# Optimization experiments

Hardware: AMD Instinct MI355X
Metric: run time of the kernel (lower is better)

## Reference

```python
import jax, jax.numpy as jnp
import numpy as np

EMBED_DIM = 256
NUM_HEADS = 8
HEAD_DIM = EMBED_DIM // NUM_HEADS
FFN_DIM = 4 * EMBED_DIM
B, N = 2, 2048


def _layernorm(x, w, b, eps=1e-5):
    mu = jnp.mean(x, axis=-1, keepdims=True)
    var = jnp.var(x, axis=-1, keepdims=True)
    return (x - mu) * jax.lax.rsqrt(var + eps) * w + b


def setup_inputs() -> dict:
    key = jax.random.key(0)
    ks = jax.random.split(key, 16)
    s = 0.02
    d = {
        "x": jax.random.normal(ks[0], (B, N, EMBED_DIM), jnp.float32),
        "influence_matrix": jax.random.uniform(ks[1], (B, N, N), jnp.float32),
        "qw": jax.random.normal(ks[2], (EMBED_DIM, EMBED_DIM), jnp.float32) * s,
        "qb": jnp.zeros((EMBED_DIM,), jnp.float32),
        "kw": jax.random.normal(ks[3], (EMBED_DIM, EMBED_DIM), jnp.float32) * s,
        "kb": jnp.zeros((EMBED_DIM,), jnp.float32),
        "vw": jax.random.normal(ks[4], (EMBED_DIM, EMBED_DIM), jnp.float32) * s,
        "vb": jnp.zeros((EMBED_DIM,), jnp.float32),
        "ow": jax.random.normal(ks[5], (EMBED_DIM, EMBED_DIM), jnp.float32) * s,
        "ob": jnp.zeros((EMBED_DIM,), jnp.float32),
        "w1": jax.random.normal(ks[6], (EMBED_DIM, FFN_DIM), jnp.float32) * s,
        "b1": jnp.zeros((FFN_DIM,), jnp.float32),
        "w2": jax.random.normal(ks[7], (FFN_DIM, EMBED_DIM), jnp.float32) * s,
        "b2": jnp.zeros((EMBED_DIM,), jnp.float32),
        "ln1_w": jnp.ones((EMBED_DIM,), jnp.float32),
        "ln1_b": jnp.zeros((EMBED_DIM,), jnp.float32),
        "ln2_w": jnp.ones((EMBED_DIM,), jnp.float32),
        "ln2_b": jnp.zeros((EMBED_DIM,), jnp.float32),
    }
    return d


def reference(x, influence_matrix, qw, qb, kw, kb, vw, vb, ow, ob,
              w1, b1, w2, b2, ln1_w, ln1_b, ln2_w, ln2_b):
    # --- pre-norm attention with multiplicative influence bias ---
    h = _layernorm(x, ln1_w, ln1_b)
    q = (h @ qw + qb).reshape(B, N, NUM_HEADS, HEAD_DIM)
    k = (h @ kw + kb).reshape(B, N, NUM_HEADS, HEAD_DIM)
    v = (h @ vw + vb).reshape(B, N, NUM_HEADS, HEAD_DIM)
    scores = jnp.einsum('bnhd,bmhd->bhnm', q, k) / np.sqrt(HEAD_DIM).astype(np.float32)
    scores = scores * (1.0 + influence_matrix[:, None, :, :])  # multiplicative bias
    attn = jax.nn.softmax(scores, axis=-1)
    out = jnp.einsum('bhnm,bmhd->bnhd', attn, v).reshape(B, N, EMBED_DIM)
    x = x + out @ ow + ob
    # --- GELU FFN (torch GELU is exact erf form) ---
    h2 = _layernorm(x, ln2_w, ln2_b)
    ff = jax.nn.gelu(h2 @ w1 + b1, approximate=False) @ w2 + b2
    return x + ff
```

## Files before the change

### kernel.cpp

```cpp
#include <hip/hip_runtime.h>
#include <hip/hip_bf16.h>
#include <math.h>

#define NSEQ 2048
#define DMODEL 256
#define STRD 296

typedef __attribute__((ext_vector_type(8))) __bf16 bf16x8;
typedef __attribute__((ext_vector_type(4))) float f32x4;
typedef __attribute__((ext_vector_type(8))) unsigned short ushort8;
typedef __attribute__((ext_vector_type(4))) unsigned int uint4e;

__device__ __forceinline__ unsigned short f2b(float f) {
    return __builtin_bit_cast(unsigned short, (__bf16)f);
}
__device__ __forceinline__ float b2f(unsigned short u) {
    return (float)__builtin_bit_cast(__bf16, u);
}
__device__ __forceinline__ bf16x8 ldfrag16(const void* p) {
    return __builtin_bit_cast(bf16x8, *(const uint4e*)p);
}
__device__ __forceinline__ uint4e pack8(float a0,float a1,float a2,float a3,
                                        float b0,float b1,float b2,float b3) {
    uint4e u;
    u.x = (unsigned)f2b(a0) | ((unsigned)f2b(a1) << 16);
    u.y = (unsigned)f2b(a2) | ((unsigned)f2b(a3) << 16);
    u.z = (unsigned)f2b(b0) | ((unsigned)f2b(b1) << 16);
    u.w = (unsigned)f2b(b2) | ((unsigned)f2b(b3) << 16);
    return u;
}

__global__ __launch_bounds__(256)
void prep_kernel(const float* __restrict__ qw, const float* __restrict__ kw,
                 const float* __restrict__ vw, const float* __restrict__ ow,
                 const float* __restrict__ w1, const float* __restrict__ w2,
                 __bf16* __restrict__ qwT, __bf16* __restrict__ kwT,
                 __bf16* __restrict__ vwT, __bf16* __restrict__ owT,
                 __bf16* __restrict__ w1T, __bf16* __restrict__ w2T)
{
    __shared__ float tile[32][33];
    const int b = blockIdx.x;
    const float* in; __bf16* out; int K, N, k0, n0;
    if (b < 256) {
        const int wsel = b >> 6, tl = b & 63;
        in  = (wsel == 0) ? qw  : (wsel == 1) ? kw  : (wsel == 2) ? vw  : ow;
        out = (wsel == 0) ? qwT : (wsel == 1) ? kwT : (wsel == 2) ? vwT : owT;
        K = 256; N = 256; k0 = (tl >> 3) * 32; n0 = (tl & 7) * 32;
    } else if (b < 512) {
        const int tl = b - 256;
        in = w1; out = w1T; K = 256; N = 1024;
        k0 = (tl >> 5) * 32; n0 = (tl & 31) * 32;
    } else {
        const int tl = b - 512;
        in = w2; out = w2T; K = 1024; N = 256;
        k0 = (tl >> 3) * 32; n0 = (tl & 7) * 32;
    }
    const int tx = threadIdx.x & 31, ty = threadIdx.x >> 5;
#pragma unroll
    for (int j = 0; j < 4; ++j)
        tile[ty * 4 + j][tx] = in[(size_t)(k0 + ty * 4 + j) * N + n0 + tx];
    __syncthreads();
#pragma unroll
    for (int j = 0; j < 4; ++j)
        out[(size_t)(n0 + ty * 4 + j) * K + k0 + tx] = (__bf16)tile[tx][ty * 4 + j];
}

__device__ __forceinline__ void stage_panel(const __bf16* __restrict__ src, int ldk,
                                            int col0, int kbase, short* dst)
{
    const int t = threadIdx.x;
#pragma unroll
    for (int i = 0; i < 8; ++i) {
        const int flat = i * 256 + t;
        const int row = flat >> 5, seg = flat & 31;
        *(uint4e*)(dst + row * STRD + seg * 8) =
            *(const uint4e*)(src + (size_t)(col0 + row) * ldk + kbase + seg * 8);
    }
}

__device__ __forceinline__ void ln_to_lds(const float* __restrict__ xrow0,
                                          const float* __restrict__ lw,
                                          const float* __restrict__ lb, short* As)
{
    const int t = threadIdx.x;
    const int r = t >> 2, q = t & 3;
    const float* xp = xrow0 + (size_t)r * 256 + q * 64;
    float4 v[16];
    float s = 0.f, s2 = 0.f;
#pragma unroll
    for (int j = 0; j < 16; ++j) {
        v[j] = *(const float4*)(xp + j * 4);
        s  += v[j].x + v[j].y + v[j].z + v[j].w;
        s2 += v[j].x*v[j].x + v[j].y*v[j].y + v[j].z*v[j].z + v[j].w*v[j].w;
    }
    s  += __shfl_xor(s, 1);  s  += __shfl_xor(s, 2);
    s2 += __shfl_xor(s2, 1); s2 += __shfl_xor(s2, 2);
    const float mu = s * (1.0f / 256.0f);
    const float rs = rsqrtf(s2 * (1.0f / 256.0f) - mu * mu + 1e-5f);
    const float* gw = lw + q * 64;
    const float* gb = lb + q * 64;
#pragma unroll
    for (int j = 0; j < 8; ++j) {
        const float4 w0 = *(const float4*)(gw + j * 8);
        const float4 w1 = *(const float4*)(gw + j * 8 + 4);
        const float4 b0 = *(const float4*)(gb + j * 8);
        const float4 b1 = *(const float4*)(gb + j * 8 + 4);
        const float4 a = v[j * 2], bq = v[j * 2 + 1];
        *(uint4e*)(As + r * STRD + q * 64 + j * 8) = pack8(
            (a.x - mu) * rs * w0.x + b0.x, (a.y - mu) * rs * w0.y + b0.y,
            (a.z - mu) * rs * w0.z + b0.z, (a.w - mu) * rs * w0.w + b0.w,
            (bq.x - mu) * rs * w1.x + b1.x, (bq.y - mu) * rs * w1.y + b1.y,
            (bq.z - mu) * rs * w1.z + b1.z, (bq.w - mu) * rs * w1.w + b1.w);
    }
}

__global__ __launch_bounds__(256)
void qkv_kernel(const float* __restrict__ x,
                const float* __restrict__ lw, const float* __restrict__ lb,
                const __bf16* __restrict__ qwT, const __bf16* __restrict__ kwT,
                const __bf16* __restrict__ vwT,
                const float* __restrict__ qb, const float* __restrict__ kb,
                const float* __restrict__ vb,
                __bf16* __restrict__ qo, __bf16* __restrict__ ko,
                __bf16* __restrict__ vto)
{
    __shared__ short As[64 * STRD];
    __shared__ short Ws[64 * STRD];
    const int z = blockIdx.z;
    const __bf16* WT  = (z == 0) ? qwT : (z == 1) ? kwT : vwT;
    const float* bias = (z == 0) ? qb  : (z == 1) ? kb  : vb;
    const int row0 = blockIdx.y * 64, col0 = blockIdx.x * 64;

    ln_to_lds(x + (size_t)row0 * 256, lw, lb, As);
    stage_panel(WT, 256, col0, 0, Ws);
    __syncthreads();

    const int t = threadIdx.x, lane = t & 63, w = t >> 6;
    const int g = lane >> 4, c = lane & 15;
    const short* ap = As + (w * 16 + c) * STRD + g * 8;
    const short* bp = Ws + c * STRD + g * 8;
    f32x4 acc[4] = {};
#pragma unroll
    for (int kc = 0; kc < 256; kc += 32) {
        const bf16x8 a = ldfrag16(ap + kc);
#pragma unroll
        for (int dt = 0; dt < 4; ++dt) {
            const bf16x8 bb = ldfrag16(bp + dt * 16 * STRD + kc);
            acc[dt] = __builtin_amdgcn_mfma_f32_16x16x32_bf16(a, bb, acc[dt], 0, 0, 0);
        }
    }

    if (z == 2) {
        __syncthreads();
        short* LT = Ws;
#pragma unroll
        for (int dt = 0; dt < 4; ++dt)
#pragma unroll
        for (int r = 0; r < 4; ++r)
            LT[(dt * 16 + c) * 72 + w * 16 + g * 4 + r] =
                (short)f2b(acc[dt][r] + bias[col0 + dt * 16 + c]);
        __syncthreads();
        const int col = t >> 2;
#pragma unroll
        for (int i = 0; i < 2; ++i) {
            const int seg = (t & 3) * 2 + i;
            *(uint4e*)(vto + (size_t)(col0 + col) * 4096 + row0 + seg * 8) =
                *(const uint4e*)&LT[col * 72 + seg * 8];
        }
    } else {
        __bf16* o = (z == 0) ? qo : ko;
#pragma unroll
        for (int dt = 0; dt < 4; ++dt)
#pragma unroll
        for (int r = 0; r < 4; ++r) {
            const int row = row0 + w * 16 + g * 4 + r;
            const int col = col0 + dt * 16 + c;
            o[(size_t)row * 256 + col] = (__bf16)(acc[dt][r] + bias[col]);
        }
    }
}

__global__ __launch_bounds__(256)
void oproj_kernel(const __bf16* __restrict__ ao, const __bf16* __restrict__ owT,
                  const float* __restrict__ ob, const float* __restrict__ x,
                  float* __restrict__ x2)
{
    __shared__ short Ws[64 * STRD];
    const int row0 = blockIdx.y * 64, col0 = blockIdx.x * 64;
    stage_panel(owT, 256, col0, 0, Ws);
    __syncthreads();
    const int t = threadIdx.x, lane = t & 63, w = t >> 6;
    const int g = lane >> 4, c = lane & 15;
    const __bf16* arow = ao + (size_t)(row0 + w * 16 + c) * 256 + g * 8;
    const short* bp = Ws + c * STRD + g * 8;
    f32x4 acc[4] = {};
#pragma unroll
    for (int kc = 0; kc < 256; kc += 32) {
        const bf16x8 a = ldfrag16(arow + kc);
#pragma unroll
        for (int dt = 0; dt < 4; ++dt) {
            const bf16x8 bb = ldfrag16(bp + dt * 16 * STRD + kc);
            acc[dt] = __builtin_amdgcn_mfma_f32_16x16x32_bf16(a, bb, acc[dt], 0, 0, 0);
        }
    }
#pragma unroll
    for (int dt = 0; dt < 4; ++dt)
#pragma unroll
    for (int r = 0; r < 4; ++r) {
        const int row = row0 + w * 16 + g * 4 + r;
        const int col = col0 + dt * 16 + c;
        x2[(size_t)row * 256 + col] =
            x[(size_t)row * 256 + col] + acc[dt][r] + ob[col];
    }
}

__global__ __launch_bounds__(256)
void ffn1_kernel(const float* __restrict__ x2,
                 const float* __restrict__ lw, const float* __restrict__ lb,
                 const __bf16* __restrict__ w1T, const float* __restrict__ b1,
                 __bf16* __restrict__ ff)
{
    __shared__ short As[64 * STRD];
    __shared__ short Ws[64 * STRD];
    const int row0 = blockIdx.y * 64, col0 = blockIdx.x * 64;
    ln_to_lds(x2 + (size_t)row0 * 256, lw, lb, As);
    stage_panel(w1T, 256, col0, 0, Ws);
    __syncthreads();
    const int t = threadIdx.x, lane = t & 63, w = t >> 6;
    const int g = lane >> 4, c = lane & 15;
    const short* ap = As + (w * 16 + c) * STRD + g * 8;
    const short* bp = Ws + c * STRD + g * 8;
    f32x4 acc[4] = {};
#pragma unroll
    for (int kc = 0; kc < 256; kc += 32) {
        const bf16x8 a = ldfrag16(ap + kc);
#pragma unroll
        for (int dt = 0; dt < 4; ++dt) {
            const bf16x8 bb = ldfrag16(bp + dt * 16 * STRD + kc);
            acc[dt] = __builtin_amdgcn_mfma_f32_16x16x32_bf16(a, bb, acc[dt], 0, 0, 0);
        }
    }
#pragma unroll
    for (int dt = 0; dt < 4; ++dt)
#pragma unroll
    for (int r = 0; r < 4; ++r) {
        const int row = row0 + w * 16 + g * 4 + r;
        const int col = col0 + dt * 16 + c;
        float val = acc[dt][r] + b1[col];
        val = 0.5f * val * (1.0f + erff(val * 0.70710678118654752f));
        ff[(size_t)row * 1024 + col] = (__bf16)val;
    }
}

__global__ __launch_bounds__(256)
void ffn2_kernel(const __bf16* __restrict__ ff, const __bf16* __restrict__ w2T,
                 const float* __restrict__ b2, const float* __restrict__ x2,
                 float* __restrict__ out)
{
    __shared__ short Ws[64 * STRD];
    const int row0 = blockIdx.y * 64, col0 = blockIdx.x * 64;
    const int t = threadIdx.x, lane = t & 63, w = t >> 6;
    const int g = lane >> 4, c = lane & 15;
    const __bf16* arow = ff + (size_t)(row0 + w * 16 + c) * 1024 + g * 8;
    const short* bp = Ws + c * STRD + g * 8;
    f32x4 acc[4] = {};
    for (int ck = 0; ck < 4; ++ck) {
        if (ck) __syncthreads();
        stage_panel(w2T, 1024, col0, ck * 256, Ws);
        __syncthreads();
#pragma unroll
        for (int kc = 0; kc < 256; kc += 32) {
            const bf16x8 a = ldfrag16(arow + ck * 256 + kc);
#pragma unroll
            for (int dt = 0; dt < 4; ++dt) {
                const bf16x8 bb = ldfrag16(bp + dt * 16 * STRD + kc);
                acc[dt] = __builtin_amdgcn_mfma_f32_16x16x32_bf16(a, bb, acc[dt], 0, 0, 0);
            }
        }
    }
#pragma unroll
    for (int dt = 0; dt < 4; ++dt)
#pragma unroll
    for (int r = 0; r < 4; ++r) {
        const int row = row0 + w * 16 + g * 4 + r;
        const int col = col0 + dt * 16 + c;
        out[(size_t)row * 256 + col] =
            x2[(size_t)row * 256 + col] + acc[dt][r] + b2[col];
    }
}

__global__ __launch_bounds__(512, 4)
void attn_kernel(const __bf16* __restrict__ Q, const __bf16* __restrict__ K,
                 const __bf16* __restrict__ VT, const float* __restrict__ infl,
                 __bf16* __restrict__ Opart, float* __restrict__ ml)
{
    __shared__ float ilds[2][16][66];
    __shared__ short Pm[8][16][104];

    const int t    = threadIdx.x;
    const int lane = t & 63;
    const int w    = t >> 6;
    const int g    = lane >> 4, c = lane & 15;
    const int b    = blockIdx.z;
    const int sp   = blockIdx.y;
    const int n0   = blockIdx.x * 16;
    const int m_start = sp * 512;
    const float scale = 0.17677669529663687f;

    const bf16x8 qf = ldfrag16(Q + (size_t)(b * NSEQ + n0 + c) * DMODEL + w * 32 + g * 8);

    const __bf16* Khead = K  + (size_t)(b * NSEQ + c) * DMODEL + w * 32 + g * 8;
    const __bf16* Vhead = VT + (size_t)(w * 32 + c) * (2 * NSEQ) + b * NSEQ + g * 8;

    const int irN = t >> 5, icol = (t & 31) * 2;
    const float* iptr = infl + (size_t)(b * NSEQ + n0 + irN) * NSEQ + icol;

    f32x4 Oacc[2] = {};
    float lsum[4] = {0.f, 0.f, 0.f, 0.f};

    float2 ireg = *(const float2*)(iptr + m_start);
    bf16x8 kf[4];
#pragma unroll
    for (int dt = 0; dt < 4; ++dt)
        kf[dt] = ldfrag16(Khead + (size_t)(m_start + dt * 16) * DMODEL);

    int buf = 0;
    for (int it = 0; it < 8; ++it) {
        const int m0 = m_start + (it << 6);
        const int mn = m_start + (((it + 1) & 7) << 6);

        *(float2*)&ilds[buf][irN][icol] = ireg;
        asm volatile("s_waitcnt lgkmcnt(0)" ::: "memory");
        __builtin_amdgcn_s_barrier();

        ireg = *(const float2*)(iptr + mn);
        bf16x8 kn[4];
#pragma unroll
        for (int dt = 0; dt < 4; ++dt)
            kn[dt] = ldfrag16(Khead + (size_t)(mn + dt * 16) * DMODEL);
        bf16x8 vf[4];
#pragma unroll
        for (int ks = 0; ks < 2; ++ks)
#pragma unroll
            for (int dt = 0; dt < 2; ++dt)
                vf[ks * 2 + dt] =
                    ldfrag16(Vhead + (size_t)(dt * 16) * (2 * NSEQ) + m0 + ks * 32);

        f32x4 s[4];
#pragma unroll
        for (int mt = 0; mt < 4; ++mt) {
            f32x4 z4 = {0.f, 0.f, 0.f, 0.f};
            s[mt] = __builtin_amdgcn_mfma_f32_16x16x32_bf16(qf, kf[mt], z4, 0, 0, 0);
        }

        float p[4][4];
#pragma unroll
        for (int mt = 0; mt < 4; ++mt)
#pragma unroll
            for (int r = 0; r < 4; ++r) {
                const float iw = scale + scale * ilds[buf][g * 4 + r][mt * 16 + c];
                const float pe = __expf(s[mt][r] * iw);
                p[mt][r] = pe;
                lsum[r] += pe;
            }
#pragma unroll
        for (int mt = 0; mt < 4; ++mt)
#pragma unroll
            for (int r = 0; r < 4; ++r)
                Pm[w][g * 4 + r][mt * 16 + c] = (short)f2b(p[mt][r]);
        asm volatile("" ::: "memory");

#pragma unroll
        for (int ks = 0; ks < 2; ++ks) {
            const bf16x8 pf = ldfrag16(&Pm[w][c][ks * 32 + g * 8]);
            Oacc[0] = __builtin_amdgcn_mfma_f32_16x16x32_bf16(pf, vf[ks * 2 + 0], Oacc[0], 0, 0, 0);
            Oacc[1] = __builtin_amdgcn_mfma_f32_16x16x32_bf16(pf, vf[ks * 2 + 1], Oacc[1], 0, 0, 0);
        }

#pragma unroll
        for (int dt = 0; dt < 4; ++dt)
            kf[dt] = kn[dt];
        buf ^= 1;
    }

#pragma unroll
    for (int off = 1; off < 16; off <<= 1)
#pragma unroll
        for (int r = 0; r < 4; ++r)
            lsum[r] += __shfl_xor(lsum[r], off);

    if (c == 0) {
#pragma unroll
        for (int r = 0; r < 4; ++r)
            ml[((size_t)(sp * 4096 + b * NSEQ + n0 + g * 4 + r)) * 8 + w] = lsum[r];
    }

#pragma unroll
    for (int r = 0; r < 4; ++r) {
        const int grow = b * NSEQ + n0 + g * 4 + r;
#pragma unroll
        for (int dt = 0; dt < 2; ++dt)
            Opart[(size_t)(sp * 4096 + grow) * 256 + w * 32 + dt * 16 + c] =
                (__bf16)Oacc[dt][r];
    }
}

__global__ __launch_bounds__(256)
void combine_kernel(const __bf16* __restrict__ Opart, const float* __restrict__ ml,
                    __bf16* __restrict__ ao)
{
    const int tid = blockIdx.x * 256 + threadIdx.x;
    const int row = tid >> 5;
    const int d0  = (tid & 31) * 8;
    const int h   = d0 >> 5;
    float l = 0.f;
#pragma unroll
    for (int sp = 0; sp < 4; ++sp)
        l += ml[((size_t)(sp * 4096 + row)) * 8 + h];
    const float inv = 1.0f / l;
    float acc[8] = {};
#pragma unroll
    for (int sp = 0; sp < 4; ++sp) {
        const ushort8 xp = *(const ushort8*)(Opart + ((size_t)(sp * 4096 + row)) * 256 + d0);
#pragma unroll
        for (int e = 0; e < 8; ++e) acc[e] += b2f(xp[e]);
    }
    __bf16 o[8];
#pragma unroll
    for (int e = 0; e < 8; ++e) o[e] = (__bf16)(acc[e] * inv);
    *(uint4e*)(ao + (size_t)row * 256 + d0) = *(uint4e*)o;
}

extern "C" void kernel_launch(void* const* d_in, const int* in_sizes, int n_in,
                              void* d_out, int out_size, void* d_ws, size_t ws_size,
                              hipStream_t stream)
{
    (void)in_sizes; (void)n_in; (void)out_size; (void)ws_size;
    const float* x    = (const float*)d_in[0];
    const float* infl = (const float*)d_in[1];
    const float* qw   = (const float*)d_in[2];
    const float* qb   = (const float*)d_in[3];
    const float* kw   = (const float*)d_in[4];
    const float* kb   = (const float*)d_in[5];
    const float* vw   = (const float*)d_in[6];
    const float* vb   = (const float*)d_in[7];
    const float* ow   = (const float*)d_in[8];
    const float* ob_  = (const float*)d_in[9];
    const float* w1   = (const float*)d_in[10];
    const float* b1   = (const float*)d_in[11];
    const float* w2   = (const float*)d_in[12];
    const float* b2   = (const float*)d_in[13];
    const float* ln1w = (const float*)d_in[14];
    const float* ln1b = (const float*)d_in[15];
    const float* ln2w = (const float*)d_in[16];
    const float* ln2b = (const float*)d_in[17];
    float* out = (float*)d_out;

    char* ws = (char*)d_ws;
    __bf16* qwT   = (__bf16*)(ws);
    __bf16* kwT   = (__bf16*)(ws + (128u << 10));
    __bf16* vwT   = (__bf16*)(ws + (256u << 10));
    __bf16* owT   = (__bf16*)(ws + (384u << 10));
    __bf16* w1T   = (__bf16*)(ws + (512u << 10));
    __bf16* w2T   = (__bf16*)(ws + (1024u << 10));
    __bf16* q     = (__bf16*)(ws +  2 * 1048576ull);
    __bf16* kx    = (__bf16*)(ws +  4 * 1048576ull);
    __bf16* vt    = (__bf16*)(ws +  6 * 1048576ull);
    __bf16* Opart = (__bf16*)(ws +  8 * 1048576ull);
    float*  mlbuf = (float*) (ws + 16 * 1048576ull);
    __bf16* ao    = (__bf16*)(ws + 17 * 1048576ull);
    float*  x2    = (float*) (ws + 19 * 1048576ull);
    __bf16* ff    = (__bf16*)(ws + 23 * 1048576ull);

    prep_kernel<<<768, 256, 0, stream>>>(qw, kw, vw, ow, w1, w2,
                                         qwT, kwT, vwT, owT, w1T, w2T);
    qkv_kernel<<<dim3(4, 64, 3), 256, 0, stream>>>(x, ln1w, ln1b, qwT, kwT, vwT,
                                                   qb, kb, vb, q, kx, vt);
    attn_kernel<<<dim3(128, 4, 2), 512, 0, stream>>>(q, kx, vt, infl, Opart, mlbuf);
    combine_kernel<<<512, 256, 0, stream>>>(Opart, mlbuf, ao);
    oproj_kernel<<<dim3(4, 64), 256, 0, stream>>>(ao, owT, ob_, x, x2);
    ffn1_kernel<<<dim3(16, 64), 256, 0, stream>>>(x2, ln2w, ln2b, w1T, b1, ff);
    ffn2_kernel<<<dim3(4, 64), 256, 0, stream>>>(ff, w2T, b2, x2, out);
}
```

Measured before the change: 238.0 us.

## Restructure pipeline: standalone LayerNorm, head-major K/V, fused combine, split-K FFN2

LayerNorm moves out of the GEMM kernels. LN1 now runs inside the prep launch and LN2 in its own kernel, and both write bf16 activations. K and V^T are stored head-major so attention reads contiguous per-head tiles. Attention drops its shared-memory influence staging and barrier and reads influence values straight into registers, using one head per wave with 256-thread blocks. The softmax combine step is folded into the output projection, GEMM row tiles shrink to 32 to raise block counts, and FFN2 becomes split-K with a separate reduction kernel. The gain is more parallelism and fewer barriers, at the cost of extra launches and more partial-sum traffic.

New measurement: 218.8 us. 8.1% less time.

```diff
diff --git a/kernel.cpp b/kernel.cpp
--- a/kernel.cpp
+++ b/kernel.cpp
@@ -3,12 +3,13 @@
 #include <math.h>
 
 #define NSEQ 2048
-#define DMODEL 256
-#define STRD 296
+#define SW 264
+#define PS 104
 
 typedef __attribute__((ext_vector_type(8))) __bf16 bf16x8;
 typedef __attribute__((ext_vector_type(4))) float f32x4;
 typedef __attribute__((ext_vector_type(8))) unsigned short ushort8;
+typedef __attribute__((ext_vector_type(4))) unsigned short ushort4e;
 typedef __attribute__((ext_vector_type(4))) unsigned int uint4e;
 
 __device__ __forceinline__ unsigned short f2b(float f) {
@@ -20,38 +21,68 @@
 __device__ __forceinline__ bf16x8 ldfrag16(const void* p) {
     return __builtin_bit_cast(bf16x8, *(const uint4e*)p);
 }
-__device__ __forceinline__ uint4e pack8(float a0,float a1,float a2,float a3,
-                                        float b0,float b1,float b2,float b3) {
-    uint4e u;
-    u.x = (unsigned)f2b(a0) | ((unsigned)f2b(a1) << 16);
-    u.y = (unsigned)f2b(a2) | ((unsigned)f2b(a3) << 16);
-    u.z = (unsigned)f2b(b0) | ((unsigned)f2b(b1) << 16);
-    u.w = (unsigned)f2b(b2) | ((unsigned)f2b(b3) << 16);
-    return u;
+
+__device__ __forceinline__ void ln_row(const float* __restrict__ x,
+                                       const float* __restrict__ g,
+                                       const float* __restrict__ b,
+                                       __bf16* __restrict__ out, int row, int lane)
+{
+    const float4 v = *(const float4*)(x + (size_t)row * 256 + lane * 4);
+    float s  = v.x + v.y + v.z + v.w;
+    float s2 = v.x*v.x + v.y*v.y + v.z*v.z + v.w*v.w;
+#pragma unroll
+    for (int off = 32; off; off >>= 1) {
+        s  += __shfl_xor(s, off);
+        s2 += __shfl_xor(s2, off);
+    }
+    const float mu = s * (1.0f / 256.0f);
+    const float rs = rsqrtf(s2 * (1.0f / 256.0f) - mu * mu + 1e-5f);
+    const float4 gv = *(const float4*)(g + lane * 4);
+    const float4 bv = *(const float4*)(b + lane * 4);
+    ushort4e o4;
+    o4.x = f2b((v.x - mu) * rs * gv.x + bv.x);
+    o4.y = f2b((v.y - mu) * rs * gv.y + bv.y);
+    o4.z = f2b((v.z - mu) * rs * gv.z + bv.z);
+    o4.w = f2b((v.w - mu) * rs * gv.w + bv.w);
+    *(ushort4e*)(out + (size_t)row * 256 + lane * 4) = o4;
+}
+
+__global__ __launch_bounds__(256)
+void ln_kernel(const float* __restrict__ x, const float* __restrict__ g,
+               const float* __restrict__ b, __bf16* __restrict__ out)
+{
+    ln_row(x, g, b, out, blockIdx.x * 4 + (threadIdx.x >> 6), threadIdx.x & 63);
 }
 
 __global__ __launch_bounds__(256)
 void prep_kernel(const float* __restrict__ qw, const float* __restrict__ kw,
                  const float* __restrict__ vw, const float* __restrict__ ow,
                  const float* __restrict__ w1, const float* __restrict__ w2,
+                 const float* __restrict__ x,
+                 const float* __restrict__ ln1w, const float* __restrict__ ln1b,
                  __bf16* __restrict__ qwT, __bf16* __restrict__ kwT,
                  __bf16* __restrict__ vwT, __bf16* __restrict__ owT,
-                 __bf16* __restrict__ w1T, __bf16* __restrict__ w2T)
+                 __bf16* __restrict__ w1T, __bf16* __restrict__ w2T,
+                 __bf16* __restrict__ h)
 {
     __shared__ float tile[32][33];
-    const int b = blockIdx.x;
+    const int bid = blockIdx.x;
+    if (bid >= 768) {
+        ln_row(x, ln1w, ln1b, h, (bid - 768) * 4 + (threadIdx.x >> 6), threadIdx.x & 63);
+        return;
+    }
     const float* in; __bf16* out; int K, N, k0, n0;
-    if (b < 256) {
-        const int wsel = b >> 6, tl = b & 63;
+    if (bid < 256) {
+        const int wsel = bid >> 6, tl = bid & 63;
         in  = (wsel == 0) ? qw  : (wsel == 1) ? kw  : (wsel == 2) ? vw  : ow;
         out = (wsel == 0) ? qwT : (wsel == 1) ? kwT : (wsel == 2) ? vwT : owT;
         K = 256; N = 256; k0 = (tl >> 3) * 32; n0 = (tl & 7) * 32;
-    } else if (b < 512) {
-        const int tl = b - 256;
+    } else if (bid < 512) {
+        const int tl = bid - 256;
         in = w1; out = w1T; K = 256; N = 1024;
         k0 = (tl >> 5) * 32; n0 = (tl & 31) * 32;
     } else {
-        const int tl = b - 512;
+        const int tl = bid - 512;
         in = w2; out = w2T; K = 1024; N = 256;
         k0 = (tl >> 3) * 32; n0 = (tl & 7) * 32;
     }
@@ -73,362 +104,312 @@
     for (int i = 0; i < 8; ++i) {
         const int flat = i * 256 + t;
         const int row = flat >> 5, seg = flat & 31;
-        *(uint4e*)(dst + row * STRD + seg * 8) =
+        *(uint4e*)(dst + row * SW + seg * 8) =
             *(const uint4e*)(src + (size_t)(col0 + row) * ldk + kbase + seg * 8);
     }
 }
 
-__device__ __forceinline__ void ln_to_lds(const float* __restrict__ xrow0,
-                                          const float* __restrict__ lw,
-                                          const float* __restrict__ lb, short* As)
-{
-    const int t = threadIdx.x;
-    const int r = t >> 2, q = t & 3;
-    const float* xp = xrow0 + (size_t)r * 256 + q * 64;
-    float4 v[16];
-    float s = 0.f, s2 = 0.f;
-#pragma unroll
-    for (int j = 0; j < 16; ++j) {
-        v[j] = *(const float4*)(xp + j * 4);
-        s  += v[j].x + v[j].y + v[j].z + v[j].w;
-        s2 += v[j].x*v[j].x + v[j].y*v[j].y + v[j].z*v[j].z + v[j].w*v[j].w;
-    }
-    s  += __shfl_xor(s, 1);  s  += __shfl_xor(s, 2);
-    s2 += __shfl_xor(s2, 1); s2 += __shfl_xor(s2, 2);
-    const float mu = s * (1.0f / 256.0f);
-    const float rs = rsqrtf(s2 * (1.0f / 256.0f) - mu * mu + 1e-5f);
-    const float* gw = lw + q * 64;
-    const float* gb = lb + q * 64;
-#pragma unroll
-    for (int j = 0; j < 8; ++j) {
-        const float4 w0 = *(const float4*)(gw + j * 8);
-        const float4 w1 = *(const float4*)(gw + j * 8 + 4);
-        const float4 b0 = *(const float4*)(gb + j * 8);
-        const float4 b1 = *(const float4*)(gb + j * 8 + 4);
-        const float4 a = v[j * 2], bq = v[j * 2 + 1];
-        *(uint4e*)(As + r * STRD + q * 64 + j * 8) = pack8(
-            (a.x - mu) * rs * w0.x + b0.x, (a.y - mu) * rs * w0.y + b0.y,
-            (a.z - mu) * rs * w0.z + b0.z, (a.w - mu) * rs * w0.w + b0.w,
-            (bq.x - mu) * rs * w1.x + b1.x, (bq.y - mu) * rs * w1.y + b1.y,
-            (bq.z - mu) * rs * w1.z + b1.z, (bq.w - mu) * rs * w1.w + b1.w);
-    }
-}
-
-__global__ __launch_bounds__(256)
-void qkv_kernel(const float* __restrict__ x,
-                const float* __restrict__ lw, const float* __restrict__ lb,
+__global__ __launch_bounds__(256)
+void qkv_kernel(const __bf16* __restrict__ h,
                 const __bf16* __restrict__ qwT, const __bf16* __restrict__ kwT,
                 const __bf16* __restrict__ vwT,
                 const float* __restrict__ qb, const float* __restrict__ kb,
                 const float* __restrict__ vb,
-                __bf16* __restrict__ qo, __bf16* __restrict__ ko,
-                __bf16* __restrict__ vto)
-{
-    __shared__ short As[64 * STRD];
-    __shared__ short Ws[64 * STRD];
+                __bf16* __restrict__ qo, __bf16* __restrict__ khm,
+                __bf16* __restrict__ vthm)
+{
+    __shared__ short Ws[64 * SW];
     const int z = blockIdx.z;
     const __bf16* WT  = (z == 0) ? qwT : (z == 1) ? kwT : vwT;
     const float* bias = (z == 0) ? qb  : (z == 1) ? kb  : vb;
-    const int row0 = blockIdx.y * 64, col0 = blockIdx.x * 64;
-
-    ln_to_lds(x + (size_t)row0 * 256, lw, lb, As);
+    const int row0 = blockIdx.y * 32, col0 = blockIdx.x * 64;
     stage_panel(WT, 256, col0, 0, Ws);
     __syncthreads();
-
     const int t = threadIdx.x, lane = t & 63, w = t >> 6;
+    const int wr = w & 1, wc = w >> 1;
     const int g = lane >> 4, c = lane & 15;
-    const short* ap = As + (w * 16 + c) * STRD + g * 8;
-    const short* bp = Ws + c * STRD + g * 8;
-    f32x4 acc[4] = {};
+    const __bf16* arow = h + (size_t)(row0 + wr * 16 + c) * 256 + g * 8;
+    const short* bp = Ws + (wc * 32 + c) * SW + g * 8;
+    f32x4 acc[2] = {};
 #pragma unroll
     for (int kc = 0; kc < 256; kc += 32) {
-        const bf16x8 a = ldfrag16(ap + kc);
-#pragma unroll
-        for (int dt = 0; dt < 4; ++dt) {
-            const bf16x8 bb = ldfrag16(bp + dt * 16 * STRD + kc);
-            acc[dt] = __builtin_amdgcn_mfma_f32_16x16x32_bf16(a, bb, acc[dt], 0, 0, 0);
-        }
-    }
-
+        const bf16x8 a  = ldfrag16(arow + kc);
+        const bf16x8 b0 = ldfrag16(bp + kc);
+        const bf16x8 b1 = ldfrag16(bp + 16 * SW + kc);
+        acc[0] = __builtin_amdgcn_mfma_f32_16x16x32_bf16(a, b0, acc[0], 0, 0, 0);
+        acc[1] = __builtin_amdgcn_mfma_f32_16x16x32_bf16(a, b1, acc[1], 0, 0, 0);
+    }
+    const int bb = row0 >> 11, nl0 = row0 & 2047;
     if (z == 2) {
         __syncthreads();
         short* LT = Ws;
 #pragma unroll
-        for (int dt = 0; dt < 4; ++dt)
-#pragma unroll
-        for (int r = 0; r < 4; ++r)
-            LT[(dt * 16 + c) * 72 + w * 16 + g * 4 + r] =
-                (short)f2b(acc[dt][r] + bias[col0 + dt * 16 + c]);
+        for (int ch = 0; ch < 2; ++ch)
+#pragma unroll
+        for (int r = 0; r < 4; ++r) {
+            const int cl = wc * 32 + ch * 16 + c;
+            LT[cl * 40 + wr * 16 + g * 4 + r] = (short)f2b(acc[ch][r] + bias[col0 + cl]);
+        }
         __syncthreads();
-        const int col = t >> 2;
-#pragma unroll
-        for (int i = 0; i < 2; ++i) {
-            const int seg = (t & 3) * 2 + i;
-            *(uint4e*)(vto + (size_t)(col0 + col) * 4096 + row0 + seg * 8) =
-                *(const uint4e*)&LT[col * 72 + seg * 8];
-        }
+        const int cl = t >> 2, seg = t & 3;
+        const int C = col0 + cl;
+        *(uint4e*)(vthm + ((size_t)((bb * 8 + (C >> 5)) * 32 + (C & 31))) * NSEQ + nl0 + seg * 8) =
+            *(const uint4e*)&LT[cl * 40 + seg * 8];
     } else {
-        __bf16* o = (z == 0) ? qo : ko;
-#pragma unroll
-        for (int dt = 0; dt < 4; ++dt)
+#pragma unroll
+        for (int ch = 0; ch < 2; ++ch)
 #pragma unroll
         for (int r = 0; r < 4; ++r) {
-            const int row = row0 + w * 16 + g * 4 + r;
-            const int col = col0 + dt * 16 + c;
-            o[(size_t)row * 256 + col] = (__bf16)(acc[dt][r] + bias[col]);
-        }
-    }
-}
-
-__global__ __launch_bounds__(256)
-void oproj_kernel(const __bf16* __restrict__ ao, const __bf16* __restrict__ owT,
-                  const float* __restrict__ ob, const float* __restrict__ x,
-                  float* __restrict__ x2)
-{
-    __shared__ short Ws[64 * STRD];
-    const int row0 = blockIdx.y * 64, col0 = blockIdx.x * 64;
-    stage_panel(owT, 256, col0, 0, Ws);
-    __syncthreads();
+            const int row = row0 + wr * 16 + g * 4 + r;
+            const int C = col0 + wc * 32 + ch * 16 + c;
+            const float val = acc[ch][r] + bias[C];
+            if (z == 0)
+                qo[(size_t)row * 256 + C] = (__bf16)val;
+            else
+                khm[((size_t)(bb * 8 + (C >> 5)) * NSEQ + (row & 2047)) * 32 + (C & 31)] = (__bf16)val;
+        }
+    }
+}
+
+__global__ __launch_bounds__(256, 4)
+void attn_kernel(const __bf16* __restrict__ Q, const __bf16* __restrict__ Khm,
+                 const __bf16* __restrict__ VThm, const float* __restrict__ infl,
+                 __bf16* __restrict__ Opart, float* __restrict__ ml)
+{
+    __shared__ short Pm[4][16 * PS];
     const int t = threadIdx.x, lane = t & 63, w = t >> 6;
     const int g = lane >> 4, c = lane & 15;
-    const __bf16* arow = ao + (size_t)(row0 + w * 16 + c) * 256 + g * 8;
-    const short* bp = Ws + c * STRD + g * 8;
-    f32x4 acc[4] = {};
+    const int qt = blockIdx.x;
+    const int hh = blockIdx.y & 1, sp = blockIdx.y >> 1;
+    const int b  = blockIdx.z;
+    const int head = hh * 4 + w;
+    const int n0 = qt * 16;
+    const int m_start = sp * 512;
+    const float scale = 0.17677669529663687f;
+
+    const bf16x8 qf = ldfrag16(Q + ((size_t)(b * NSEQ + n0 + c)) * 256 + head * 32 + g * 8);
+    const __bf16* Kh = Khm + ((size_t)(b * 8 + head)) * NSEQ * 32 + g * 8;
+    const __bf16* Vh = VThm + ((size_t)(b * 8 + head)) * 32 * NSEQ + g * 8;
+    const float* ib = infl + ((size_t)(b * NSEQ + n0 + g * 4)) * NSEQ + c;
+
+    f32x4 Oacc[2] = {};
+    float lsum[4] = {0.f, 0.f, 0.f, 0.f};
+
+    bf16x8 kf[4];
+    float finf[4][4];
+#pragma unroll
+    for (int mt = 0; mt < 4; ++mt) {
+        kf[mt] = ldfrag16(Kh + (size_t)(m_start + mt * 16 + c) * 32);
+#pragma unroll
+        for (int r = 0; r < 4; ++r)
+            finf[mt][r] = ib[(size_t)r * NSEQ + m_start + mt * 16];
+    }
+
+    for (int it = 0; it < 8; ++it) {
+        const int m0 = m_start + (it << 6);
+        const int mn = m_start + (((it + 1) & 7) << 6);
+
+        f32x4 s[4];
+#pragma unroll
+        for (int mt = 0; mt < 4; ++mt) {
+            f32x4 z4 = {0.f, 0.f, 0.f, 0.f};
+            s[mt] = __builtin_amdgcn_mfma_f32_16x16x32_bf16(qf, kf[mt], z4, 0, 0, 0);
+        }
+#pragma unroll
+        for (int mt = 0; mt < 4; ++mt)
+            kf[mt] = ldfrag16(Kh + (size_t)(mn + mt * 16 + c) * 32);
+        bf16x8 vf[4];
+#pragma unroll
+        for (int ks = 0; ks < 2; ++ks)
+#pragma unroll
+        for (int dt = 0; dt < 2; ++dt)
+            vf[ks * 2 + dt] = ldfrag16(Vh + (size_t)(dt * 16 + c) * NSEQ + m0 + ks * 32);
+
+        float p[4][4];
+#pragma unroll
+        for (int mt = 0; mt < 4; ++mt)
+#pragma unroll
+        for (int r = 0; r < 4; ++r) {
+            const float pe = __expf(s[mt][r] * (scale + scale * finf[mt][r]));
+            p[mt][r] = pe;
+            lsum[r] += pe;
+        }
+#pragma unroll
+        for (int mt = 0; mt < 4; ++mt)
+#pragma unroll
+        for (int r = 0; r < 4; ++r)
+            finf[mt][r] = ib[(size_t)r * NSEQ + mn + mt * 16];
+
+        short* pmw = Pm[w];
+#pragma unroll
+        for (int mt = 0; mt < 4; ++mt)
+#pragma unroll
+        for (int r = 0; r < 4; ++r)
+            pmw[(g * 4 + r) * PS + mt * 16 + c] = (short)f2b(p[mt][r]);
+        asm volatile("" ::: "memory");
+
+#pragma unroll
+        for (int ks = 0; ks < 2; ++ks) {
+            const bf16x8 pf = ldfrag16(pmw + c * PS + ks * 32 + g * 8);
+            Oacc[0] = __builtin_amdgcn_mfma_f32_16x16x32_bf16(pf, vf[ks * 2 + 0], Oacc[0], 0, 0, 0);
+            Oacc[1] = __builtin_amdgcn_mfma_f32_16x16x32_bf16(pf, vf[ks * 2 + 1], Oacc[1], 0, 0, 0);
+        }
+    }
+
+#pragma unroll
+    for (int off = 1; off < 16; off <<= 1)
+#pragma unroll
+        for (int r = 0; r < 4; ++r)
+            lsum[r] += __shfl_xor(lsum[r], off);
+    if (c == 0) {
+#pragma unroll
+        for (int r = 0; r < 4; ++r)
+            ml[((size_t)sp * 4096 + b * NSEQ + n0 + g * 4 + r) * 8 + head] = lsum[r];
+    }
+#pragma unroll
+    for (int r = 0; r < 4; ++r) {
+        const size_t grow = (size_t)sp * 4096 + b * NSEQ + n0 + g * 4 + r;
+#pragma unroll
+        for (int dt = 0; dt < 2; ++dt)
+            Opart[grow * 256 + head * 32 + dt * 16 + c] = (__bf16)Oacc[dt][r];
+    }
+}
+
+__global__ __launch_bounds__(256)
+void oproj_kernel(const __bf16* __restrict__ Opart, const float* __restrict__ ml,
+                  const __bf16* __restrict__ owT, const float* __restrict__ ob,
+                  const float* __restrict__ x, float* __restrict__ x2)
+{
+    __shared__ short Ws[64 * SW];
+    const int row0 = blockIdx.y * 32, col0 = blockIdx.x * 64;
+    stage_panel(owT, 256, col0, 0, Ws);
+    const int t = threadIdx.x, lane = t & 63, w = t >> 6;
+    const int wr = w & 1, wc = w >> 1;
+    const int g = lane >> 4, c = lane & 15;
+    const int row = row0 + wr * 16 + c;
+    float linv[8];
+#pragma unroll
+    for (int hh = 0; hh < 8; ++hh) {
+        float l = 0.f;
+#pragma unroll
+        for (int sp = 0; sp < 4; ++sp)
+            l += ml[((size_t)sp * 4096 + row) * 8 + hh];
+        linv[hh] = 1.0f / l;
+    }
+    __syncthreads();
+    const short* bp = Ws + (wc * 32 + c) * SW + g * 8;
+    f32x4 acc[2] = {};
 #pragma unroll
     for (int kc = 0; kc < 256; kc += 32) {
-        const bf16x8 a = ldfrag16(arow + kc);
-#pragma unroll
-        for (int dt = 0; dt < 4; ++dt) {
-            const bf16x8 bb = ldfrag16(bp + dt * 16 * STRD + kc);
-            acc[dt] = __builtin_amdgcn_mfma_f32_16x16x32_bf16(a, bb, acc[dt], 0, 0, 0);
-        }
-    }
-#pragma unroll
-    for (int dt = 0; dt < 4; ++dt)
+        const int hsel = kc >> 5;
+        float av[8] = {};
+#pragma unroll
+        for (int sp = 0; sp < 4; ++sp) {
+            const ushort8 o8 = *(const ushort8*)(Opart + ((size_t)sp * 4096 + row) * 256 + kc + g * 8);
+#pragma unroll
+            for (int e = 0; e < 8; ++e) av[e] += b2f(o8[e]);
+        }
+        ushort8 a8;
+#pragma unroll
+        for (int e = 0; e < 8; ++e) a8[e] = f2b(av[e] * linv[hsel]);
+        const bf16x8 a  = __builtin_bit_cast(bf16x8, a8);
+        const bf16x8 b0 = ldfrag16(bp + kc);
+        const bf16x8 b1 = ldfrag16(bp + 16 * SW + kc);
+        acc[0] = __builtin_amdgcn_mfma_f32_16x16x32_bf16(a, b0, acc[0], 0, 0, 0);
+        acc[1] = __builtin_amdgcn_mfma_f32_16x16x32_bf16(a, b1, acc[1], 0, 0, 0);
+    }
+#pragma unroll
+    for (int ch = 0; ch < 2; ++ch)
 #pragma unroll
     for (int r = 0; r < 4; ++r) {
-        const int row = row0 + w * 16 + g * 4 + r;
-        const int col = col0 + dt * 16 + c;
-        x2[(size_t)row * 256 + col] =
-            x[(size_t)row * 256 + col] + acc[dt][r] + ob[col];
-    }
-}
-
-__global__ __launch_bounds__(256)
-void ffn1_kernel(const float* __restrict__ x2,
-                 const float* __restrict__ lw, const float* __restrict__ lb,
-                 const __bf16* __restrict__ w1T, const float* __restrict__ b1,
-                 __bf16* __restrict__ ff)
-{
-    __shared__ short As[64 * STRD];
-    __shared__ short Ws[64 * STRD];
-    const int row0 = blockIdx.y * 64, col0 = blockIdx.x * 64;
-    ln_to_lds(x2 + (size_t)row0 * 256, lw, lb, As);
+        const int rr = row0 + wr * 16 + g * 4 + r;
+        const int C = col0 + wc * 32 + ch * 16 + c;
+        x2[(size_t)rr * 256 + C] = x[(size_t)rr * 256 + C] + acc[ch][r] + ob[C];
+    }
+}
+
+__global__ __launch_bounds__(256)
+void ffn1_kernel(const __bf16* __restrict__ h2, const __bf16* __restrict__ w1T,
+                 const float* __restrict__ b1, __bf16* __restrict__ ff)
+{
+    __shared__ short Ws[64 * SW];
+    const int row0 = blockIdx.y * 32, col0 = blockIdx.x * 64;
     stage_panel(w1T, 256, col0, 0, Ws);
     __syncthreads();
     const int t = threadIdx.x, lane = t & 63, w = t >> 6;
+    const int wr = w & 1, wc = w >> 1;
     const int g = lane >> 4, c = lane & 15;
-    const short* ap = As + (w * 16 + c) * STRD + g * 8;
-    const short* bp = Ws + c * STRD + g * 8;
-    f32x4 acc[4] = {};
+    const __bf16* arow = h2 + (size_t)(row0 + wr * 16 + c) * 256 + g * 8;
+    const short* bp = Ws + (wc * 32 + c) * SW + g * 8;
+    f32x4 acc[2] = {};
 #pragma unroll
     for (int kc = 0; kc < 256; kc += 32) {
-        const bf16x8 a = ldfrag16(ap + kc);
-#pragma unroll
-        for (int dt = 0; dt < 4; ++dt) {
-            const bf16x8 bb = ldfrag16(bp + dt * 16 * STRD + kc);
-            acc[dt] = __builtin_amdgcn_mfma_f32_16x16x32_bf16(a, bb, acc[dt], 0, 0, 0);
-        }
-    }
-#pragma unroll
-    for (int dt = 0; dt < 4; ++dt)
+        const bf16x8 a  = ldfrag16(arow + kc);
+        const bf16x8 b0 = ldfrag16(bp + kc);
+        const bf16x8 b1 = ldfrag16(bp + 16 * SW + kc);
+        acc[0] = __builtin_amdgcn_mfma_f32_16x16x32_bf16(a, b0, acc[0], 0, 0, 0);
+        acc[1] = __builtin_amdgcn_mfma_f32_16x16x32_bf16(a, b1, acc[1], 0, 0, 0);
+    }
+#pragma unroll
+    for (int ch = 0; ch < 2; ++ch)
 #pragma unroll
     for (int r = 0; r < 4; ++r) {
-        const int row = row0 + w * 16 + g * 4 + r;
-        const int col = col0 + dt * 16 + c;
-        float val = acc[dt][r] + b1[col];
+        const int row = row0 + wr * 16 + g * 4 + r;
+        const int C = col0 + wc * 32 + ch * 16 + c;
+        float val = acc[ch][r] + b1[C];
         val = 0.5f * val * (1.0f + erff(val * 0.70710678118654752f));
-        ff[(size_t)row * 1024 + col] = (__bf16)val;
-    }
-}
-
-__global__ __launch_bounds__(256)
-void ffn2_kernel(const __bf16* __restrict__ ff, const __bf16* __restrict__ w2T,
-                 const float* __restrict__ b2, const float* __restrict__ x2,
-                 float* __restrict__ out)
-{
-    __shared__ short Ws[64 * STRD];
-    const int row0 = blockIdx.y * 64, col0 = blockIdx.x * 64;
+        ff[(size_t)row * 1024 + C] = (__bf16)val;
+    }
+}
+
+__global__ __launch_bounds__(256)
+void ffn2p_kernel(const __bf16* __restrict__ ff, const __bf16* __restrict__ w2T,
+                  __bf16* __restrict__ fpart)
+{
+    __shared__ short Ws[64 * SW];
+    const int sp = blockIdx.z;
+    const int row0 = blockIdx.y * 32, col0 = blockIdx.x * 64;
+    stage_panel(w2T, 1024, col0, sp * 256, Ws);
+    __syncthreads();
     const int t = threadIdx.x, lane = t & 63, w = t >> 6;
+    const int wr = w & 1, wc = w >> 1;
     const int g = lane >> 4, c = lane & 15;
-    const __bf16* arow = ff + (size_t)(row0 + w * 16 + c) * 1024 + g * 8;
-    const short* bp = Ws + c * STRD + g * 8;
-    f32x4 acc[4] = {};
-    for (int ck = 0; ck < 4; ++ck) {
-        if (ck) __syncthreads();
-        stage_panel(w2T, 1024, col0, ck * 256, Ws);
-        __syncthreads();
-#pragma unroll
-        for (int kc = 0; kc < 256; kc += 32) {
-            const bf16x8 a = ldfrag16(arow + ck * 256 + kc);
-#pragma unroll
-            for (int dt = 0; dt < 4; ++dt) {
-                const bf16x8 bb = ldfrag16(bp + dt * 16 * STRD + kc);
-                acc[dt] = __builtin_amdgcn_mfma_f32_16x16x32_bf16(a, bb, acc[dt], 0, 0, 0);
-            }
-        }
-    }
-#pragma unroll
-    for (int dt = 0; dt < 4; ++dt)
+    const __bf16* arow = ff + (size_t)(row0 + wr * 16 + c) * 1024 + sp * 256 + g * 8;
+    const short* bp = Ws + (wc * 32 + c) * SW + g * 8;
+    f32x4 acc[2] = {};
+#pragma unroll
+    for (int kc = 0; kc < 256; kc += 32) {
+        const bf16x8 a  = ldfrag16(arow + kc);
+        const bf16x8 b0 = ldfrag16(bp + kc);
+        const bf16x8 b1 = ldfrag16(bp + 16 * SW + kc);
+        acc[0] = __builtin_amdgcn_mfma_f32_16x16x32_bf16(a, b0, acc[0], 0, 0, 0);
+        acc[1] = __builtin_amdgcn_mfma_f32_16x16x32_bf16(a, b1, acc[1], 0, 0, 0);
+    }
+#pragma unroll
+    for (int ch = 0; ch < 2; ++ch)
 #pragma unroll
     for (int r = 0; r < 4; ++r) {
-        const int row = row0 + w * 16 + g * 4 + r;
-        const int col = col0 + dt * 16 + c;
-        out[(size_t)row * 256 + col] =
-            x2[(size_t)row * 256 + col] + acc[dt][r] + b2[col];
-    }
-}
-
-__global__ __launch_bounds__(512, 4)
-void attn_kernel(const __bf16* __restrict__ Q, const __bf16* __restrict__ K,
-                 const __bf16* __restrict__ VT, const float* __restrict__ infl,
-                 __bf16* __restrict__ Opart, float* __restrict__ ml)
-{
-    __shared__ float ilds[2][16][66];
-    __shared__ short Pm[8][16][104];
-
-    const int t    = threadIdx.x;
-    const int lane = t & 63;
-    const int w    = t >> 6;
-    const int g    = lane >> 4, c = lane & 15;
-    const int b    = blockIdx.z;
-    const int sp   = blockIdx.y;
-    const int n0   = blockIdx.x * 16;
-    const int m_start = sp * 512;
-    const float scale = 0.17677669529663687f;
-
-    const bf16x8 qf = ldfrag16(Q + (size_t)(b * NSEQ + n0 + c) * DMODEL + w * 32 + g * 8);
-
-    const __bf16* Khead = K  + (size_t)(b * NSEQ + c) * DMODEL + w * 32 + g * 8;
-    const __bf16* Vhead = VT + (size_t)(w * 32 + c) * (2 * NSEQ) + b * NSEQ + g * 8;
-
-    const int irN = t >> 5, icol = (t & 31) * 2;
-    const float* iptr = infl + (size_t)(b * NSEQ + n0 + irN) * NSEQ + icol;
-
-    f32x4 Oacc[2] = {};
-    float lsum[4] = {0.f, 0.f, 0.f, 0.f};
-
-    float2 ireg = *(const float2*)(iptr + m_start);
-    bf16x8 kf[4];
-#pragma unroll
-    for (int dt = 0; dt < 4; ++dt)
-        kf[dt] = ldfrag16(Khead + (size_t)(m_start + dt * 16) * DMODEL);
-
-    int buf = 0;
-    for (int it = 0; it < 8; ++it) {
-        const int m0 = m_start + (it << 6);
-        const int mn = m_start + (((it + 1) & 7) << 6);
-
-        *(float2*)&ilds[buf][irN][icol] = ireg;
-        asm volatile("s_waitcnt lgkmcnt(0)" ::: "memory");
-        __builtin_amdgcn_s_barrier();
-
-        ireg = *(const float2*)(iptr + mn);
-        bf16x8 kn[4];
-#pragma unroll
-        for (int dt = 0; dt < 4; ++dt)
-            kn[dt] = ldfrag16(Khead + (size_t)(mn + dt * 16) * DMODEL);
-        bf16x8 vf[4];
-#pragma unroll
-        for (int ks = 0; ks < 2; ++ks)
-#pragma unroll
-            for (int dt = 0; dt < 2; ++dt)
-                vf[ks * 2 + dt] =
-                    ldfrag16(Vhead + (size_t)(dt * 16) * (2 * NSEQ) + m0 + ks * 32);
-
-        f32x4 s[4];
-#pragma unroll
-        for (int mt = 0; mt < 4; ++mt) {
-            f32x4 z4 = {0.f, 0.f, 0.f, 0.f};
-            s[mt] = __builtin_amdgcn_mfma_f32_16x16x32_bf16(qf, kf[mt], z4, 0, 0, 0);
-        }
-
-        float p[4][4];
-#pragma unroll
-        for (int mt = 0; mt < 4; ++mt)
-#pragma unroll
-            for (int r = 0; r < 4; ++r) {
-                const float iw = scale + scale * ilds[buf][g * 4 + r][mt * 16 + c];
-                const float pe = __expf(s[mt][r] * iw);
-                p[mt][r] = pe;
-                lsum[r] += pe;
-            }
-#pragma unroll
-        for (int mt = 0; mt < 4; ++mt)
-#pragma unroll
-            for (int r = 0; r < 4; ++r)
-                Pm[w][g * 4 + r][mt * 16 + c] = (short)f2b(p[mt][r]);
-        asm volatile("" ::: "memory");
-
-#pragma unroll
-        for (int ks = 0; ks < 2; ++ks) {
-            const bf16x8 pf = ldfrag16(&Pm[w][c][ks * 32 + g * 8]);
-            Oacc[0] = __builtin_amdgcn_mfma_f32_16x16x32_bf16(pf, vf[ks * 2 + 0], Oacc[0], 0, 0, 0);
-            Oacc[1] = __builtin_amdgcn_mfma_f32_16x16x32_bf16(pf, vf[ks * 2 + 1], Oacc[1], 0, 0, 0);
-        }
-
-#pragma unroll
-        for (int dt = 0; dt < 4; ++dt)
-            kf[dt] = kn[dt];
-        buf ^= 1;
-    }
-
-#pragma unroll
-    for (int off = 1; off < 16; off <<= 1)
-#pragma unroll
-        for (int r = 0; r < 4; ++r)
-            lsum[r] += __shfl_xor(lsum[r], off);
-
-    if (c == 0) {
-#pragma unroll
-        for (int r = 0; r < 4; ++r)
-            ml[((size_t)(sp * 4096 + b * NSEQ + n0 + g * 4 + r)) * 8 + w] = lsum[r];
-    }
-
-#pragma unroll
-    for (int r = 0; r < 4; ++r) {
-        const int grow = b * NSEQ + n0 + g * 4 + r;
-#pragma unroll
-        for (int dt = 0; dt < 2; ++dt)
-            Opart[(size_t)(sp * 4096 + grow) * 256 + w * 32 + dt * 16 + c] =
-                (__bf16)Oacc[dt][r];
-    }
-}
-
-__global__ __launch_bounds__(256)
-void combine_kernel(const __bf16* __restrict__ Opart, const float* __restrict__ ml,
-                    __bf16* __restrict__ ao)
-{
-    const int tid = blockIdx.x * 256 + threadIdx.x;
-    const int row = tid >> 5;
-    const int d0  = (tid & 31) * 8;
-    const int h   = d0 >> 5;
-    float l = 0.f;
-#pragma unroll
-    for (int sp = 0; sp < 4; ++sp)
-        l += ml[((size_t)(sp * 4096 + row)) * 8 + h];
-    const float inv = 1.0f / l;
-    float acc[8] = {};
+        const int row = row0 + wr * 16 + g * 4 + r;
+        const int C = col0 + wc * 32 + ch * 16 + c;
+        fpart[((size_t)sp * 4096 + row) * 256 + C] = (__bf16)acc[ch][r];
+    }
+}
+
+__global__ __launch_bounds__(256)
+void ffn2r_kernel(const __bf16* __restrict__ fpart, const float* __restrict__ x2,
+                  const float* __restrict__ b2, float* __restrict__ out)
+{
+    const int i4 = (blockIdx.x * 256 + threadIdx.x) * 4;
+    const int col = i4 & 255;
+    float4 o = *(const float4*)(x2 + i4);
+    const float4 bb = *(const float4*)(b2 + col);
+    o.x += bb.x; o.y += bb.y; o.z += bb.z; o.w += bb.w;
 #pragma unroll
     for (int sp = 0; sp < 4; ++sp) {
-        const ushort8 xp = *(const ushort8*)(Opart + ((size_t)(sp * 4096 + row)) * 256 + d0);
-#pragma unroll
-        for (int e = 0; e < 8; ++e) acc[e] += b2f(xp[e]);
-    }
-    __bf16 o[8];
-#pragma unroll
-    for (int e = 0; e < 8; ++e) o[e] = (__bf16)(acc[e] * inv);
-    *(uint4e*)(ao + (size_t)row * 256 + d0) = *(uint4e*)o;
+        const ushort4e p4 = *(const ushort4e*)(fpart + (size_t)sp * 1048576 + i4);
+        o.x += b2f(p4.x); o.y += b2f(p4.y); o.z += b2f(p4.z); o.w += b2f(p4.w);
+    }
+    *(float4*)(out + i4) = o;
 }
 
 extern "C" void kernel_launch(void* const* d_in, const int* in_sizes, int n_in,
@@ -463,22 +444,25 @@
     __bf16* owT   = (__bf16*)(ws + (384u << 10));
     __bf16* w1T   = (__bf16*)(ws + (512u << 10));
     __bf16* w2T   = (__bf16*)(ws + (1024u << 10));
-    __bf16* q     = (__bf16*)(ws +  2 * 1048576ull);
-    __bf16* kx    = (__bf16*)(ws +  4 * 1048576ull);
-    __bf16* vt    = (__bf16*)(ws +  6 * 1048576ull);
-    __bf16* Opart = (__bf16*)(ws +  8 * 1048576ull);
-    float*  mlbuf = (float*) (ws + 16 * 1048576ull);
-    __bf16* ao    = (__bf16*)(ws + 17 * 1048576ull);
-    float*  x2    = (float*) (ws + 19 * 1048576ull);
-    __bf16* ff    = (__bf16*)(ws + 23 * 1048576ull);
-
-    prep_kernel<<<768, 256, 0, stream>>>(qw, kw, vw, ow, w1, w2,
-                                         qwT, kwT, vwT, owT, w1T, w2T);
-    qkv_kernel<<<dim3(4, 64, 3), 256, 0, stream>>>(x, ln1w, ln1b, qwT, kwT, vwT,
-                                                   qb, kb, vb, q, kx, vt);
-    attn_kernel<<<dim3(128, 4, 2), 512, 0, stream>>>(q, kx, vt, infl, Opart, mlbuf);
-    combine_kernel<<<512, 256, 0, stream>>>(Opart, mlbuf, ao);
-    oproj_kernel<<<dim3(4, 64), 256, 0, stream>>>(ao, owT, ob_, x, x2);
-    ffn1_kernel<<<dim3(16, 64), 256, 0, stream>>>(x2, ln2w, ln2b, w1T, b1, ff);
-    ffn2_kernel<<<dim3(4, 64), 256, 0, stream>>>(ff, w2T, b2, x2, out);
-}
+    float*  mlbuf = (float*) (ws + (1536u << 10));
+    __bf16* h     = (__bf16*)(ws +  2 * 1048576ull);
+    __bf16* q     = (__bf16*)(ws +  4 * 1048576ull);
+    __bf16* khm   = (__bf16*)(ws +  6 * 1048576ull);
+    __bf16* vthm  = (__bf16*)(ws +  8 * 1048576ull);
+    __bf16* Opart = (__bf16*)(ws + 10 * 1048576ull);
+    float*  x2    = (float*) (ws +  4 * 1048576ull);
+    __bf16* h2    = (__bf16*)(ws +  8 * 1048576ull);
+    __bf16* ff    = (__bf16*)(ws + 10 * 1048576ull);
+    __bf16* fpart = (__bf16*)(ws + 18 * 1048576ull);
+
+    prep_kernel<<<1792, 256, 0, stream>>>(qw, kw, vw, ow, w1, w2, x, ln1w, ln1b,
+                                          qwT, kwT, vwT, owT, w1T, w2T, h);
+    qkv_kernel<<<dim3(4, 128, 3), 256, 0, stream>>>(h, qwT, kwT, vwT, qb, kb, vb,
+                                                    q, khm, vthm);
+    attn_kernel<<<dim3(128, 8, 2), 256, 0, stream>>>(q, khm, vthm, infl, Opart, mlbuf);
+    oproj_kernel<<<dim3(4, 128), 256, 0, stream>>>(Opart, mlbuf, owT, ob_, x, x2);
+    ln_kernel<<<1024, 256, 0, stream>>>(x2, ln2w, ln2b, h2);
+    ffn1_kernel<<<dim3(16, 128), 256, 0, stream>>>(h2, w1T, b1, ff);
+    ffn2p_kernel<<<dim3(4, 128, 4), 256, 0, stream>>>(ff, w2T, fpart);
+    ffn2r_kernel<<<1024, 256, 0, stream>>>(fpart, x2, b2, out);
+}
```
